# Performance work log

Measured on AMD Instinct MI355X. Metric: run time of the kernel, lower is better.

Reference implementation:

```python
import jax, jax.numpy as jnp
import numpy as np
from jax import lax

HARD_RANK = 5
HARD_PROB = 0.5
MARGIN = 0.0
EPS = 1e-6  # F.pairwise_distance default eps (added to the difference)


def setup_inputs() -> dict:
    key = jax.random.key(0)
    x = jax.random.normal(key, (8192, 2, 256), dtype=jnp.float32)
    return {"x": x}


def _l2norm(v):
    # torch F.normalize: v / max(||v||, 1e-12)
    n = jnp.sqrt(jnp.sum(v * v, axis=1, keepdims=True))
    return v / jnp.maximum(n, 1e-12)


def reference(x):
    B, _, D = x.shape
    a = _l2norm(x[:, 0, :])  # anchors, unit norm -> ||a_i||^2 = 1
    p = _l2norm(x[:, 1, :])  # positives, unit norm

    # Full anchor-vs-positive distance matrix via GEMM (no [B,B,D] tensor).
    # torch pairwise_distance uses ||a - p + eps||, expand exactly:
    # ||a-p+eps*1||^2 = ||a||^2 + ||p||^2 - 2 a.p + 2*eps*(sum(a)-sum(p)) + D*eps^2
    am = lax.stop_gradient(a)
    pm = lax.stop_gradient(p)
    ip = am @ pm.T                          # [B, B]
    ra = jnp.sum(am, axis=1)                # [B]
    rp = jnp.sum(pm, axis=1)                # [B]
    d2 = 2.0 - 2.0 * ip + 2.0 * EPS * (ra[:, None] - rp[None, :]) + D * EPS * EPS
    dist = jnp.sqrt(jnp.maximum(d2, 0.0))

    # Exclude self (excidx drops idx) by masking diagonal to +inf.
    dmine = jnp.where(jnp.eye(B, dtype=bool), jnp.inf, dist)

    # hard_rank smallest distances per row (rank 0 = hardest negative).
    _, top_idx = lax.top_k(-dmine, HARD_RANK)   # [B, HARD_RANK]

    # With prob hard_prob pick the hardest; else uniform among top hard_rank.
    kr = jax.random.key(1)
    k1, k2 = jax.random.split(kr)
    coin = jax.random.uniform(k1, (B,)) < HARD_PROB
    rand_rank = jax.random.randint(k2, (B,), 0, HARD_RANK)
    rank = jnp.where(coin, 0, rand_rank)
    negidx = top_idx[jnp.arange(B), rank]       # [B]

    neg = p[negidx, :]
    pos_d2 = jnp.sum(jnp.square(a - p + EPS), axis=1)
    neg_d2 = jnp.sum(jnp.square(a - neg + EPS), axis=1)
    return jnp.mean(jax.nn.relu(pos_d2 - neg_d2 + MARGIN))
```

## Files before the change

### kernel.cpp

```cpp
#include <hip/hip_runtime.h>
#include <hip/hip_bf16.h>
#include <stdint.h>


#define NB 8192
#define NCG 32
#define EPSF 1e-6f
#define IMIN (-2147483647 - 1)

typedef int i32x4 __attribute__((ext_vector_type(4)));

struct U2 { uint32_t x, y; };

__host__ __device__ __forceinline__ uint32_t rotl32(uint32_t v, int n) {
  return (v << n) | (v >> (32 - n));
}

__host__ __device__ __forceinline__ U2 tf2x32(uint32_t k0, uint32_t k1,
                                              uint32_t x0, uint32_t x1) {
  uint32_t k2 = k0 ^ k1 ^ 0x1BD11BDAu;
#define TF_R(r) { x0 += x1; x1 = rotl32(x1, r); x1 ^= x0; }
  x0 += k0; x1 += k1;
  TF_R(13) TF_R(15) TF_R(26) TF_R(6)
  x0 += k1; x1 += k2 + 1u;
  TF_R(17) TF_R(29) TF_R(16) TF_R(24)
  x0 += k2; x1 += k0 + 2u;
  TF_R(13) TF_R(15) TF_R(26) TF_R(6)
  x0 += k0; x1 += k1 + 3u;
  TF_R(17) TF_R(29) TF_R(16) TF_R(24)
  x0 += k1; x1 += k2 + 4u;
  TF_R(13) TF_R(15) TF_R(26) TF_R(6)
  x0 += k2; x1 += k0 + 5u;
#undef TF_R
  U2 r; r.x = x0; r.y = x1; return r;
}

__device__ __forceinline__ uint32_t rng_word(U2 r) { return r.x ^ r.y; }

#define FINS5I(T0, T1, T2, T3, T4, C) {           \
    const int _c = (C), _t0 = T0, _t1 = T1, _t2 = T2, _t3 = T3, _t4 = T4; \
    T0 = _t0 > _c ? _t0 : _c;                     \
    asm("v_med3_i32 %0, %1, %2, %3" : "=v"(T1) : "v"(_c), "v"(_t0), "v"(_t1)); \
    asm("v_med3_i32 %0, %1, %2, %3" : "=v"(T2) : "v"(_c), "v"(_t1), "v"(_t2)); \
    asm("v_med3_i32 %0, %1, %2, %3" : "=v"(T3) : "v"(_c), "v"(_t2), "v"(_t3)); \
    asm("v_med3_i32 %0, %1, %2, %3" : "=v"(T4) : "v"(_c), "v"(_t3), "v"(_t4)); }

#define FINS5C(T0, T1, T2, T3, T4, C) {           \
    const int _t0 = T0, _t1 = T1, _t2 = T2, _t3 = T3, _t4 = T4, _c = C; \
    T0 = _t0 > _c ? _t0 : _c;                     \
    { const int m = _c < _t0 ? _c : _t0; T1 = _t1 > m ? _t1 : m; } \
    { const int m = _c < _t1 ? _c : _t1; T2 = _t2 > m ? _t2 : m; } \
    { const int m = _c < _t2 ? _c : _t2; T3 = _t3 > m ? _t3 : m; } \
    { const int m = _c < _t3 ? _c : _t3; T4 = _t4 > m ? _t4 : m; } }

__device__ __forceinline__ void gload16(const void* g, void* l) {
  __builtin_amdgcn_global_load_lds(
      (const __attribute__((address_space(1))) unsigned int*)g,
      (__attribute__((address_space(3))) unsigned int*)l, 16, 0, 0);
}

__global__ __launch_bounds__(256) void prep_kernel(
    const float* __restrict__ x,
    char* __restrict__ aq8, char* __restrict__ pq8) {
  const int w = threadIdx.x >> 6, l = threadIdx.x & 63;
  const int row = blockIdx.x * 4 + w;
  const float4* xr = (const float4*)(x + (size_t)row * 512);
  const float4 a4 = xr[l];
  const float4 p4 = xr[64 + l];
  float sa = a4.x * a4.x + a4.y * a4.y + a4.z * a4.z + a4.w * a4.w;
  float sp = p4.x * p4.x + p4.y * p4.y + p4.z * p4.z + p4.w * p4.w;
#pragma unroll
  for (int off = 32; off; off >>= 1) { sa += __shfl_xor(sa, off); sp += __shfl_xor(sp, off); }
  const float ia = 127.0f / fmaxf(sqrtf(sa), 1e-12f);
  const float ip_ = 127.0f / fmaxf(sqrtf(sp), 1e-12f);
  const int qa0 = (int)rintf(a4.x * ia), qa1 = (int)rintf(a4.y * ia);
  const int qa2 = (int)rintf(a4.z * ia), qa3 = (int)rintf(a4.w * ia);
  const int qp0 = (int)rintf(p4.x * ip_), qp1 = (int)rintf(p4.y * ip_);
  const int qp2 = (int)rintf(p4.z * ip_), qp3 = (int)rintf(p4.w * ip_);
  const uint32_t ua = (qa0 & 255) | ((qa1 & 255) << 8) |
                      ((qa2 & 255) << 16) | ((uint32_t)(qa3 & 255) << 24);
  const uint32_t up = (qp0 & 255) | ((qp1 & 255) << 8) |
                      ((qp2 & 255) << 16) | ((uint32_t)(qp3 & 255) << 24);
  *(uint32_t*)(aq8 + (size_t)row * 256 + l * 4) = ua;
  *(uint32_t*)(pq8 + (size_t)row * 256 + l * 4) = up;
}

__global__ __launch_bounds__(512, 2) void dist_topk_kernel(
    const char* __restrict__ aq8, const char* __restrict__ pq8,
    int* __restrict__ part) {
  __shared__ __align__(16) char smem[49152];

  const int tid = threadIdx.x;
  const int w = tid >> 6, l = tid & 63;
  const int lo = l & 15, hi = l >> 4;
  const int wr = w >> 2, wc = w & 3;

  const int b = blockIdx.x;
  const int xcd = b & 7, j = b >> 3;
  const int rb = (xcd >> 1) * 16 + (j >> 4);
  const int cb = (xcd & 1) * 16 + (j & 15);
  const int row0 = rb * 128, col0 = cb * 256;
  const bool hasDiag = (cb == (rb >> 1));

  i32x4 acc[4][4];
#pragma unroll
  for (int aq = 0; aq < 4; ++aq)
#pragma unroll
    for (int pq = 0; pq < 4; ++pq) { i32x4 z = {0, 0, 0, 0}; acc[aq][pq] = z; }

#define STAGE(BUF, KS)                                                        \
  {                                                                           \
    { const int off = tid * 16;                                               \
      const int R = off >> 7;                                                 \
      const int s = ((off >> 4) & 7) ^ (R & 7);                               \
      const int r = 2 * R + (s >> 2);                                         \
      const int kb = (s & 3) * 16;                                            \
      gload16(aq8 + (size_t)(row0 + r) * 256 + (KS) * 64 + kb,                \
              smem + (BUF) * 24576 + off); }                                  \
    _Pragma("unroll")                                                         \
    for (int jj = 0; jj < 2; ++jj) {                                          \
      const int off = jj * 8192 + tid * 16;                                   \
      const int R = off >> 7;                                                 \
      const int s = ((off >> 4) & 7) ^ (R & 7);                               \
      const int c = 2 * R + (s >> 2);                                         \
      const int kb = (s & 3) * 16;                                            \
      gload16(pq8 + (size_t)(col0 + c) * 256 + (KS) * 64 + kb,                \
              smem + (BUF) * 24576 + 8192 + off); }                           \
  }

#define LADDR(RR, T) (((RR) >> 1) * 128 + (((((RR) & 1) * 4 + (T)) ^ (((RR) >> 1) & 7)) * 16))

#define COMPUTE(BUF)                                                          \
  {                                                                           \
    i32x4 aF0, aF1, aF2, aF3, bF0, bF1, bF2, bF3;                             \
    { const int r = wr * 64 + 0 + lo;                                         \
      aF0 = __builtin_bit_cast(i32x4, *(const uint4*)(smem + (BUF) * 24576 + LADDR(r, hi))); } \
    { const int r = wr * 64 + 16 + lo;                                        \
      aF1 = __builtin_bit_cast(i32x4, *(const uint4*)(smem + (BUF) * 24576 + LADDR(r, hi))); } \
    { const int r = wr * 64 + 32 + lo;                                        \
      aF2 = __builtin_bit_cast(i32x4, *(const uint4*)(smem + (BUF) * 24576 + LADDR(r, hi))); } \
    { const int r = wr * 64 + 48 + lo;                                        \
      aF3 = __builtin_bit_cast(i32x4, *(const uint4*)(smem + (BUF) * 24576 + LADDR(r, hi))); } \
    { const int c = wc * 64 + 0 + lo;                                         \
      bF0 = __builtin_bit_cast(i32x4, *(const uint4*)(smem + (BUF) * 24576 + 8192 + LADDR(c, hi))); } \
    { const int c = wc * 64 + 16 + lo;                                        \
      bF1 = __builtin_bit_cast(i32x4, *(const uint4*)(smem + (BUF) * 24576 + 8192 + LADDR(c, hi))); } \
    __builtin_amdgcn_s_setprio(1);                                            \
    acc[0][0] = __builtin_amdgcn_mfma_i32_16x16x64_i8(bF0, aF0, acc[0][0], 0, 0, 0); \
    acc[1][0] = __builtin_amdgcn_mfma_i32_16x16x64_i8(bF0, aF1, acc[1][0], 0, 0, 0); \
    acc[2][0] = __builtin_amdgcn_mfma_i32_16x16x64_i8(bF0, aF2, acc[2][0], 0, 0, 0); \
    acc[3][0] = __builtin_amdgcn_mfma_i32_16x16x64_i8(bF0, aF3, acc[3][0], 0, 0, 0); \
    { const int c = wc * 64 + 32 + lo;                                        \
      bF2 = __builtin_bit_cast(i32x4, *(const uint4*)(smem + (BUF) * 24576 + 8192 + LADDR(c, hi))); } \
    acc[0][1] = __builtin_amdgcn_mfma_i32_16x16x64_i8(bF1, aF0, acc[0][1], 0, 0, 0); \
    acc[1][1] = __builtin_amdgcn_mfma_i32_16x16x64_i8(bF1, aF1, acc[1][1], 0, 0, 0); \
    acc[2][1] = __builtin_amdgcn_mfma_i32_16x16x64_i8(bF1, aF2, acc[2][1], 0, 0, 0); \
    acc[3][1] = __builtin_amdgcn_mfma_i32_16x16x64_i8(bF1, aF3, acc[3][1], 0, 0, 0); \
    { const int c = wc * 64 + 48 + lo;                                        \
      bF3 = __builtin_bit_cast(i32x4, *(const uint4*)(smem + (BUF) * 24576 + 8192 + LADDR(c, hi))); } \
    acc[0][2] = __builtin_amdgcn_mfma_i32_16x16x64_i8(bF2, aF0, acc[0][2], 0, 0, 0); \
    acc[1][2] = __builtin_amdgcn_mfma_i32_16x16x64_i8(bF2, aF1, acc[1][2], 0, 0, 0); \
    acc[2][2] = __builtin_amdgcn_mfma_i32_16x16x64_i8(bF2, aF2, acc[2][2], 0, 0, 0); \
    acc[3][2] = __builtin_amdgcn_mfma_i32_16x16x64_i8(bF2, aF3, acc[3][2], 0, 0, 0); \
    acc[0][3] = __builtin_amdgcn_mfma_i32_16x16x64_i8(bF3, aF0, acc[0][3], 0, 0, 0); \
    acc[1][3] = __builtin_amdgcn_mfma_i32_16x16x64_i8(bF3, aF1, acc[1][3], 0, 0, 0); \
    acc[2][3] = __builtin_amdgcn_mfma_i32_16x16x64_i8(bF3, aF2, acc[2][3], 0, 0, 0); \
    acc[3][3] = __builtin_amdgcn_mfma_i32_16x16x64_i8(bF3, aF3, acc[3][3], 0, 0, 0); \
    __builtin_amdgcn_s_setprio(0);                                            \
  }

#define WAITV3 { asm volatile("s_waitcnt vmcnt(3)" ::: "memory"); }
#define WAITV0 { asm volatile("s_waitcnt vmcnt(0)" ::: "memory"); }
#define BAR    { __builtin_amdgcn_s_barrier(); }

  STAGE(0, 0)
  STAGE(1, 1) WAITV3 BAR COMPUTE(0) BAR
  STAGE(0, 2) WAITV3 BAR COMPUTE(1) BAR
  STAGE(1, 3) WAITV3 BAR COMPUTE(0) BAR
  WAITV0 BAR COMPUTE(1)

#undef STAGE
#undef LADDR
#undef COMPUTE
#undef WAITV3
#undef WAITV0
#undef BAR

  __syncthreads();
  int* mls = (int*)smem;
  const int vb13 = 8191 - (col0 + wc * 64) - hi * 4;
#pragma unroll
  for (int aq = 0; aq < 4; ++aq) {
    int T0 = IMIN, T1 = IMIN, T2 = IMIN, T3 = IMIN, T4 = IMIN;
    const int arow = row0 + wr * 64 + aq * 16 + lo;
#pragma unroll
    for (int pq = 0; pq < 4; ++pq)
#pragma unroll
      for (int rr = 0; rr < 4; ++rr) {
        int key = (int)(((uint32_t)acc[aq][pq][rr]) << 13) + vb13 - (pq * 16 + rr);
        if (hasDiag) {
          if (col0 + wc * 64 + pq * 16 + hi * 4 + rr == arow) key = IMIN;
        }
        FINS5I(T0, T1, T2, T3, T4, key);
      }
    int* dst = mls + (wr * 64 + aq * 16 + lo) * 81 + (wc * 4 + hi) * 5;
    dst[0] = T0; dst[1] = T1; dst[2] = T2; dst[3] = T3; dst[4] = T4;
  }
  __syncthreads();

  if (tid < 256) {
    const int row = tid >> 1, half = tid & 1;
    const int* s2 = mls + row * 81 + half * 40;
    int M0 = IMIN, M1 = IMIN, M2 = IMIN, M3 = IMIN, M4 = IMIN;
#pragma unroll
    for (int k = 0; k < 40; ++k) FINS5I(M0, M1, M2, M3, M4, s2[k]);
    const int c0 = __shfl_xor(M0, 1), c1 = __shfl_xor(M1, 1),
              c2 = __shfl_xor(M2, 1), c3 = __shfl_xor(M3, 1),
              c4 = __shfl_xor(M4, 1);
    FINS5I(M0, M1, M2, M3, M4, c0);
    FINS5I(M0, M1, M2, M3, M4, c1);
    FINS5I(M0, M1, M2, M3, M4, c2);
    FINS5I(M0, M1, M2, M3, M4, c3);
    FINS5I(M0, M1, M2, M3, M4, c4);
    if (half == 0) {
      int* dst = part + ((size_t)(row0 + row) * NCG + cb) * 5;
      dst[0] = M0; dst[1] = M1; dst[2] = M2; dst[3] = M3; dst[4] = M4;
    }
  }
}

__global__ __launch_bounds__(256) void merge_loss_kernel(
    const float* __restrict__ x, const int* __restrict__ part,
    float* __restrict__ rowloss,
    uint32_t k1a, uint32_t k1b, uint32_t k2a, uint32_t k2b) {
  const int w = threadIdx.x >> 6, l = threadIdx.x & 63;
  const int i = blockIdx.x * 4 + w;
  __shared__ int cs[4][160];
  const int* src = part + (size_t)i * (NCG * 5);
  cs[w][l] = src[l];
  cs[w][64 + l] = src[64 + l];
  if (l < 32) cs[w][128 + l] = src[128 + l];
  __syncthreads();

  int T0 = IMIN, T1 = IMIN, T2 = IMIN, T3 = IMIN, T4 = IMIN;
  for (int rch = 0; rch < NCG; ++rch) {
    for (int q = 0; q < 5; ++q) {
      const int c = cs[w][rch * 5 + q];
      if (c <= T4) break;
      FINS5C(T0, T1, T2, T3, T4, c);
    }
  }

  const uint32_t cw = rng_word(tf2x32(k1a, k1b, 0u, (uint32_t)i));
  const bool coin = (cw >> 31) == 0u;
  const uint32_t hb = rng_word(tf2x32(k2a, k2b, 0u, (uint32_t)i));
  const uint32_t lb = rng_word(tf2x32(k2a, k2b, 0u, (uint32_t)(NB + i)));
  const int rr = (int)(((hb % 5u) + (lb % 5u)) % 5u);
  const int rank = coin ? 0 : rr;
  const int kch = (rank == 0) ? T0 : (rank == 1) ? T1 : (rank == 2) ? T2
                : (rank == 3) ? T3 : T4;
  const int neg = 8191 - (kch & 8191);

  const float4 xa = *(const float4*)(x + (size_t)i * 512 + l * 4);
  const float4 xp = *(const float4*)(x + (size_t)i * 512 + 256 + l * 4);
  const float4 xn = *(const float4*)(x + (size_t)neg * 512 + 256 + l * 4);
  float sa = xa.x * xa.x + xa.y * xa.y + xa.z * xa.z + xa.w * xa.w;
  float sp = xp.x * xp.x + xp.y * xp.y + xp.z * xp.z + xp.w * xp.w;
  float sn = xn.x * xn.x + xn.y * xn.y + xn.z * xn.z + xn.w * xn.w;
#pragma unroll
  for (int off = 32; off; off >>= 1) {
    sa += __shfl_xor(sa, off); sp += __shfl_xor(sp, off); sn += __shfl_xor(sn, off);
  }
  const float na = fmaxf(sqrtf(sa), 1e-12f);
  const float np = fmaxf(sqrtf(sp), 1e-12f);
  const float nn = fmaxf(sqrtf(sn), 1e-12f);

  float pos = 0.f, ng = 0.f;
  {
    float av, pv, nv, dp, dn;
    av = xa.x / na; pv = xp.x / np; nv = xn.x / nn;
    dp = av - pv + EPSF; pos += dp * dp; dn = av - nv + EPSF; ng += dn * dn;
    av = xa.y / na; pv = xp.y / np; nv = xn.y / nn;
    dp = av - pv + EPSF; pos += dp * dp; dn = av - nv + EPSF; ng += dn * dn;
    av = xa.z / na; pv = xp.z / np; nv = xn.z / nn;
    dp = av - pv + EPSF; pos += dp * dp; dn = av - nv + EPSF; ng += dn * dn;
    av = xa.w / na; pv = xp.w / np; nv = xn.w / nn;
    dp = av - pv + EPSF; pos += dp * dp; dn = av - nv + EPSF; ng += dn * dn;
  }
#pragma unroll
  for (int off = 32; off; off >>= 1) {
    pos += __shfl_xor(pos, off); ng += __shfl_xor(ng, off);
  }
  if (l == 0) rowloss[i] = fmaxf(pos - ng, 0.0f);
}

__global__ __launch_bounds__(256) void finalize_kernel(
    const float* __restrict__ rowloss, float* __restrict__ out) {
  __shared__ float s[256];
  const int t = threadIdx.x;
  float a = 0.f;
  for (int k = 0; k < NB / 256; ++k) a += rowloss[t + 256 * k];
  s[t] = a;
  __syncthreads();
  for (int h = 128; h; h >>= 1) {
    if (t < h) s[t] += s[t + h];
    __syncthreads();
  }
  if (t == 0) out[0] = s[0] / (float)NB;
}

extern "C" void kernel_launch(void* const* d_in, const int* in_sizes, int n_in,
                              void* d_out, int out_size, void* d_ws, size_t ws_size,
                              hipStream_t stream) {
  (void)in_sizes; (void)n_in; (void)out_size; (void)ws_size;
  const float* x = (const float*)d_in[0];
  float* out = (float*)d_out;
  char* ws = (char*)d_ws;

  char* aq8 = ws;
  char* pq8 = ws + (size_t)2 * 1024 * 1024;
  int* part = (int*)(ws + (size_t)4 * 1024 * 1024);
  float* rowloss = (float*)(ws + (size_t)4 * 1024 * 1024 +
                            (size_t)NB * NCG * 5 * sizeof(int));

  U2 c0 = tf2x32(0u, 1u, 0u, 0u);
  U2 c1 = tf2x32(0u, 1u, 0u, 1u);
  const uint32_t k1a = c0.x, k1b = c0.y;
  const uint32_t k2a = c1.x, k2b = c1.y;

  prep_kernel<<<NB / 4, 256, 0, stream>>>(x, aq8, pq8);
  dist_topk_kernel<<<2048, 512, 0, stream>>>(aq8, pq8, part);
  merge_loss_kernel<<<NB / 4, 256, 0, stream>>>(x, part, rowloss, k1a, k1b, k2a, k2b);
  finalize_kernel<<<1, 256, 0, stream>>>(rowloss, out);
}
```

Measured before the change: 60.19 us.

## Triple-buffer K stages in LDS and specialize diagonal top-k loop

LDS grows from two to three 24KB stage buffers. The next stage's global loads are now issued before computing the current stage, and one barrier per iteration is dropped, so loads overlap MFMA work with less synchronisation. The top-5 mining loop is duplicated into diagonal and non-diagonal versions, so the diagonal check is hoisted out of the inner loop. The larger LDS footprint (72KB per block with launch bounds 512,2) may limit occupancy, and removing barriers depends on the three-buffer rotation preventing write-after-read hazards.

```diff
diff --git a/kernel.cpp b/kernel.cpp
--- a/kernel.cpp
+++ b/kernel.cpp
@@ -88,7 +88,7 @@
 __global__ __launch_bounds__(512, 2) void dist_topk_kernel(
     const char* __restrict__ aq8, const char* __restrict__ pq8,
     int* __restrict__ part) {
-  __shared__ __align__(16) char smem[49152];
+  __shared__ __align__(16) char smem[73728];
 
   const int tid = threadIdx.x;
   const int w = tid >> 6, l = tid & 63;
@@ -174,10 +174,11 @@
 #define BAR    { __builtin_amdgcn_s_barrier(); }
 
   STAGE(0, 0)
-  STAGE(1, 1) WAITV3 BAR COMPUTE(0) BAR
-  STAGE(0, 2) WAITV3 BAR COMPUTE(1) BAR
-  STAGE(1, 3) WAITV3 BAR COMPUTE(0) BAR
-  WAITV0 BAR COMPUTE(1)
+  STAGE(1, 1)
+  WAITV3 BAR STAGE(2, 2) COMPUTE(0)
+  WAITV3 BAR STAGE(0, 3) COMPUTE(1)
+  WAITV3 BAR COMPUTE(2)
+  WAITV0 BAR COMPUTE(0)
 
 #undef STAGE
 #undef LADDR
@@ -189,23 +190,28 @@
   __syncthreads();
   int* mls = (int*)smem;
   const int vb13 = 8191 - (col0 + wc * 64) - hi * 4;
-#pragma unroll
-  for (int aq = 0; aq < 4; ++aq) {
-    int T0 = IMIN, T1 = IMIN, T2 = IMIN, T3 = IMIN, T4 = IMIN;
-    const int arow = row0 + wr * 64 + aq * 16 + lo;
-#pragma unroll
-    for (int pq = 0; pq < 4; ++pq)
-#pragma unroll
-      for (int rr = 0; rr < 4; ++rr) {
-        int key = (int)(((uint32_t)acc[aq][pq][rr]) << 13) + vb13 - (pq * 16 + rr);
-        if (hasDiag) {
-          if (col0 + wc * 64 + pq * 16 + hi * 4 + rr == arow) key = IMIN;
-        }
-        FINS5I(T0, T1, T2, T3, T4, key);
-      }
-    int* dst = mls + (wr * 64 + aq * 16 + lo) * 81 + (wc * 4 + hi) * 5;
-    dst[0] = T0; dst[1] = T1; dst[2] = T2; dst[3] = T3; dst[4] = T4;
-  }
+
+#define MINE_LOOP(DIAG)                                                       \
+  _Pragma("unroll")                                                           \
+  for (int aq = 0; aq < 4; ++aq) {                                            \
+    int T0 = IMIN, T1 = IMIN, T2 = IMIN, T3 = IMIN, T4 = IMIN;                \
+    const int arow = row0 + wr * 64 + aq * 16 + lo;                           \
+    _Pragma("unroll")                                                         \
+    for (int pq = 0; pq < 4; ++pq)                                            \
+      _Pragma("unroll")                                                       \
+      for (int rr = 0; rr < 4; ++rr) {                                        \
+        int key = (int)(((uint32_t)acc[aq][pq][rr]) << 13) + vb13 - (pq * 16 + rr); \
+        if (DIAG) {                                                           \
+          if (col0 + wc * 64 + pq * 16 + hi * 4 + rr == arow) key = IMIN;     \
+        }                                                                     \
+        FINS5I(T0, T1, T2, T3, T4, key);                                      \
+      }                                                                       \
+    int* dst = mls + (wr * 64 + aq * 16 + lo) * 81 + (wc * 4 + hi) * 5;       \
+    dst[0] = T0; dst[1] = T1; dst[2] = T2; dst[3] = T3; dst[4] = T4;          \
+  }
+
+  if (hasDiag) { MINE_LOOP(true) } else { MINE_LOOP(false) }
+#undef MINE_LOOP
   __syncthreads();
 
   if (tid < 256) {
```

After: 59.30 us (median of 2 runs). About the same (-1.5%).
